# Kernel optimization log

Hardware: AMD Instinct MI355X
Metric: run time of the kernel (lower is better)

The kernel has to match this reference:

```python
import jax, jax.numpy as jnp
import numpy as np

STD = 0.5      # wrapper's self.std used as the noise sampling std
EPS = 1e-12    # BERT LayerNorm eps
NOISE_SEED = 42


def setup_inputs() -> dict:
    key = jax.random.key(0)
    ks = jax.random.split(key, 8)
    B, S, H, V, P, T = 32, 512, 768, 30522, 512, 2
    return {
        "input_ids": jax.random.randint(ks[0], (B, S), 0, V, dtype=jnp.int32),
        "token_type_ids": jnp.zeros((B, S), dtype=jnp.int32),
        "importance_scores": jax.random.uniform(ks[1], (B, S), dtype=jnp.float32),
        "word_emb": jax.random.normal(ks[2], (V, H), dtype=jnp.float32) * 0.02,
        "pos_emb": jax.random.normal(ks[3], (P, H), dtype=jnp.float32) * 0.02,
        "type_emb": jax.random.normal(ks[4], (T, H), dtype=jnp.float32) * 0.02,
        "ln_gamma": jnp.ones((H,), dtype=jnp.float32),
        "ln_beta": jnp.zeros((H,), dtype=jnp.float32),
    }


def _layernorm(x, g, b):
    mu = x.mean(-1, keepdims=True)
    var = ((x - mu) ** 2).mean(-1, keepdims=True)
    return (x - mu) * jax.lax.rsqrt(var + EPS) * g + b


def reference(input_ids, token_type_ids, importance_scores, word_emb, pos_emb,
              type_emb, ln_gamma, ln_beta):
    B, S = input_ids.shape
    # BERT embeddings: word + position + token_type, then LayerNorm (dropout=eval/no-op)
    emb = word_emb[input_ids] + pos_emb[:S][None, :, :] + type_emb[token_type_ids]
    x = _layernorm(emb, ln_gamma, ln_beta)  # [B,S,H]

    # min-max normalize importance scores per sequence (inf handled as in original)
    smax = importance_scores.max(axis=1, keepdims=True)
    tmp = jnp.where(jnp.isinf(importance_scores), 99.0, importance_scores)
    smin = tmp.min(axis=1, keepdims=True)
    norm = (importance_scores - smin) / (smax - smin)
    norm = jnp.where(importance_scores.sum() == 0, importance_scores, norm)

    finite = jnp.isfinite(importance_scores)
    score = jnp.where(finite, norm, 0.0)      # -inf positions masked out below
    score = score.at[:, 0].set(1.0)           # CLS token forced to importance 1
    mask = finite.at[:, 0].set(True)

    # soft_suff: sigma = 1 - importance; noise ~ N(0, STD); x += noise * sigma * x
    sigma = (1.0 - score) * mask.astype(x.dtype)          # [B,S]
    noise = jax.random.normal(jax.random.key(NOISE_SEED), x.shape, dtype=x.dtype) * STD
    x = x + noise * sigma[:, :, None] * jax.lax.stop_gradient(x)
    return x
```

## Files before the change

kernel.cpp:

```cpp
#include <hip/hip_runtime.h>
#include <hip/hip_bf16.h>
#include <math.h>

#define Hh   768
#define Ss   512
#define Bb   32
#define NTOK (Bb * Ss)
#define NTOT (NTOK * Hh)

__device__ __forceinline__ void tfr(unsigned &x0, unsigned &x1, int r) {
  x0 += x1;
  x1 = (x1 << r) | (x1 >> (32 - r));
  x1 ^= x0;
}

__device__ __forceinline__ uint2 threefry_0_42(unsigned x0, unsigned x1) {
  const unsigned ks0 = 0u, ks1 = 42u, ks2 = 0x1BD11BF0u;
  x0 += ks0; x1 += ks1;
  tfr(x0, x1, 13); tfr(x0, x1, 15); tfr(x0, x1, 26); tfr(x0, x1, 6);
  x0 += ks1; x1 += ks2 + 1u;
  tfr(x0, x1, 17); tfr(x0, x1, 29); tfr(x0, x1, 16); tfr(x0, x1, 24);
  x0 += ks2; x1 += ks0 + 2u;
  tfr(x0, x1, 13); tfr(x0, x1, 15); tfr(x0, x1, 26); tfr(x0, x1, 6);
  x0 += ks0; x1 += ks1 + 3u;
  tfr(x0, x1, 17); tfr(x0, x1, 29); tfr(x0, x1, 16); tfr(x0, x1, 24);
  x0 += ks1; x1 += ks2 + 4u;
  tfr(x0, x1, 13); tfr(x0, x1, 15); tfr(x0, x1, 26); tfr(x0, x1, 6);
  x0 += ks2; x1 += ks0 + 5u;
  return make_uint2(x0, x1);
}

__device__ __forceinline__ float erfinv_xla(float x) {
  float w = -log1pf(-x * x);
  float p;
  if (w < 5.0f) {
    w = w - 2.5f;
    p = 2.81022636e-08f;
    p = fmaf(p, w, 3.43273939e-07f);
    p = fmaf(p, w, -3.5233877e-06f);
    p = fmaf(p, w, -4.39150654e-06f);
    p = fmaf(p, w, 0.00021858087f);
    p = fmaf(p, w, -0.00125372503f);
    p = fmaf(p, w, -0.00417768164f);
    p = fmaf(p, w, 0.246640727f);
    p = fmaf(p, w, 1.50140941f);
  } else {
    w = sqrtf(w) - 3.0f;
    p = -0.000200214257f;
    p = fmaf(p, w, 0.000100950558f);
    p = fmaf(p, w, 0.00134934322f);
    p = fmaf(p, w, -0.00367342844f);
    p = fmaf(p, w, 0.00573950773f);
    p = fmaf(p, w, -0.0076224613f);
    p = fmaf(p, w, 0.00943887047f);
    p = fmaf(p, w, 1.00167406f);
    p = fmaf(p, w, 2.83297682f);
  }
  return p * x;
}

__device__ __forceinline__ float noise_at(unsigned i) {
  uint2 r = threefry_0_42(0u, i);
  unsigned bits = r.x ^ r.y;
  float f = __uint_as_float((bits >> 9) | 0x3F800000u) - 1.0f;
  const float LO = -0.99999994f;
  float u = fmaxf(LO, f * 2.0f + LO);
  return 1.41421354f * erfinv_xla(u) * 0.5f;
}

__global__ __launch_bounds__(512) void row_stats_kernel(
    const float* __restrict__ imp, float* __restrict__ ws) {
  int b = blockIdx.x;
  int tid = threadIdx.x;
  float v = imp[b * Ss + tid];
  float vmax = v;
  float vmin = isinf(v) ? 99.0f : v;
  float vsum = v;
  for (int o = 32; o > 0; o >>= 1) {
    vmax = fmaxf(vmax, __shfl_down(vmax, o));
    vmin = fminf(vmin, __shfl_down(vmin, o));
    vsum += __shfl_down(vsum, o);
  }
  __shared__ float smax[8], smin[8], ssum[8];
  int wave = tid >> 6, lane = tid & 63;
  if (lane == 0) { smax[wave] = vmax; smin[wave] = vmin; ssum[wave] = vsum; }
  __syncthreads();
  if (tid == 0) {
    float a = smax[0], m = smin[0], c = ssum[0];
    for (int w = 1; w < 8; ++w) {
      a = fmaxf(a, smax[w]); m = fminf(m, smin[w]); c += ssum[w];
    }
    ws[b] = a; ws[32 + b] = m; ws[64 + b] = c;
  }
}

__global__ __launch_bounds__(256) void bert_embed_ln_noise_kernel(
    const int* __restrict__ ids, const int* __restrict__ tts,
    const float* __restrict__ imp,
    const float* __restrict__ wemb, const float* __restrict__ pemb,
    const float* __restrict__ temb, const float* __restrict__ gamma,
    const float* __restrict__ beta, const float* __restrict__ stats,
    float* __restrict__ out) {
  const int t = blockIdx.x;
  const int b = t >> 9;
  const int s = t & 511;
  const int tid = threadIdx.x;

  const int id = ids[t];
  const int tt = tts[t];
  const float* wr = wemb + (size_t)id * Hh;
  const float* pr = pemb + (size_t)s * Hh;
  const float* tr = temb + (size_t)tt * Hh;

  float e0 = wr[tid]       + pr[tid]       + tr[tid];
  float e1 = wr[tid + 256] + pr[tid + 256] + tr[tid + 256];
  float e2 = wr[tid + 512] + pr[tid + 512] + tr[tid + 512];

  __shared__ float red[4];
  __shared__ float sh_sigma;
  const int wave = tid >> 6, lane = tid & 63;

  float ps = e0 + e1 + e2;
  for (int o = 32; o > 0; o >>= 1) ps += __shfl_down(ps, o);
  if (lane == 0) red[wave] = ps;
  __syncthreads();
  const float mu = (red[0] + red[1] + red[2] + red[3]) * (1.0f / Hh);
  __syncthreads();

  const float d0 = e0 - mu, d1 = e1 - mu, d2 = e2 - mu;
  float pv = d0 * d0 + d1 * d1 + d2 * d2;
  for (int o = 32; o > 0; o >>= 1) pv += __shfl_down(pv, o);
  if (lane == 0) red[wave] = pv;

  if (tid == 0) {
    float total = 0.0f;
    for (int w = 0; w < 32; ++w) total += stats[64 + w];
    const float score = imp[t];
    float sig = 0.0f;
    if (s != 0) {
      const bool fin = isfinite(score);
      const float mx = stats[b], mn = stats[32 + b];
      const float val = (total == 0.0f) ? score : (score - mn) / (mx - mn);
      const float sc = fin ? val : 0.0f;
      sig = fin ? (1.0f - sc) : 0.0f;
    }
    sh_sigma = sig;
  }
  __syncthreads();
  const float var = (red[0] + red[1] + red[2] + red[3]) * (1.0f / Hh);
  const float rstd = rsqrtf(var + 1e-12f);
  const float sig = sh_sigma;

  const float y0 = d0 * rstd * gamma[tid]       + beta[tid];
  const float y1 = d1 * rstd * gamma[tid + 256] + beta[tid + 256];
  const float y2 = d2 * rstd * gamma[tid + 512] + beta[tid + 512];

  const unsigned base = (unsigned)t * Hh;
  const float n0 = noise_at(base + tid);
  const float n1 = noise_at(base + tid + 256);
  const float n2 = noise_at(base + tid + 512);

  out[base + tid]       = fmaf(n0 * sig, y0, y0);
  out[base + tid + 256] = fmaf(n1 * sig, y1, y1);
  out[base + tid + 512] = fmaf(n2 * sig, y2, y2);
}

extern "C" void kernel_launch(void* const* d_in, const int* in_sizes, int n_in,
                              void* d_out, int out_size, void* d_ws, size_t ws_size,
                              hipStream_t stream) {
  const int*   ids   = (const int*)d_in[0];
  const int*   tts   = (const int*)d_in[1];
  const float* imp   = (const float*)d_in[2];
  const float* wemb  = (const float*)d_in[3];
  const float* pemb  = (const float*)d_in[4];
  const float* temb  = (const float*)d_in[5];
  const float* gamma = (const float*)d_in[6];
  const float* beta  = (const float*)d_in[7];
  float* out   = (float*)d_out;
  float* stats = (float*)d_ws;

  row_stats_kernel<<<Bb, Ss, 0, stream>>>(imp, stats);
  bert_embed_ln_noise_kernel<<<NTOK, 256, 0, stream>>>(
      ids, tts, imp, wemb, pemb, temb, gamma, beta, stats, out);
}
```

Baseline: 197.4 us.

## Vectorize embedding LN kernel with float4, 192 threads, hoisted noise generation

Each thread now handles four contiguous hidden elements through float4 loads and stores, with 192 threads per token block instead of 256. The Threefry noise and erfinv are computed before the reductions so they can overlap the memory latency. Threefry is specialised for key 0, the log1p is replaced by the fast __logf, and the sqrt(2)*std scale is folded into sigma. The fast log may change noise values slightly versus the XLA reference, and the 3-wave block shape changes occupancy.

Measured after the change: 173.6 us. 12.1% less time.

```diff
diff --git a/kernel.cpp b/kernel.cpp
--- a/kernel.cpp
+++ b/kernel.cpp
@@ -1,12 +1,11 @@
 #include <hip/hip_runtime.h>
-#include <hip/hip_bf16.h>
 #include <math.h>
 
 #define Hh   768
 #define Ss   512
 #define Bb   32
 #define NTOK (Bb * Ss)
-#define NTOT (NTOK * Hh)
+#define NT   192
 
 __device__ __forceinline__ void tfr(unsigned &x0, unsigned &x1, int r) {
   x0 += x1;
@@ -14,27 +13,30 @@
   x1 ^= x0;
 }
 
-__device__ __forceinline__ uint2 threefry_0_42(unsigned x0, unsigned x1) {
-  const unsigned ks0 = 0u, ks1 = 42u, ks2 = 0x1BD11BF0u;
-  x0 += ks0; x1 += ks1;
-  tfr(x0, x1, 13); tfr(x0, x1, 15); tfr(x0, x1, 26); tfr(x0, x1, 6);
+__device__ __forceinline__ unsigned tf_bits_0_42(unsigned ctr) {
+  const unsigned ks1 = 42u, ks2 = 0x1BD11BF0u;
+  unsigned x0 = 0u, x1 = ctr + ks1;
+  tfr(x0,x1,13); tfr(x0,x1,15); tfr(x0,x1,26); tfr(x0,x1,6);
   x0 += ks1; x1 += ks2 + 1u;
-  tfr(x0, x1, 17); tfr(x0, x1, 29); tfr(x0, x1, 16); tfr(x0, x1, 24);
-  x0 += ks2; x1 += ks0 + 2u;
-  tfr(x0, x1, 13); tfr(x0, x1, 15); tfr(x0, x1, 26); tfr(x0, x1, 6);
-  x0 += ks0; x1 += ks1 + 3u;
-  tfr(x0, x1, 17); tfr(x0, x1, 29); tfr(x0, x1, 16); tfr(x0, x1, 24);
+  tfr(x0,x1,17); tfr(x0,x1,29); tfr(x0,x1,16); tfr(x0,x1,24);
+  x0 += ks2; x1 += 2u;
+  tfr(x0,x1,13); tfr(x0,x1,15); tfr(x0,x1,26); tfr(x0,x1,6);
+  x1 += ks1 + 3u;
+  tfr(x0,x1,17); tfr(x0,x1,29); tfr(x0,x1,16); tfr(x0,x1,24);
   x0 += ks1; x1 += ks2 + 4u;
-  tfr(x0, x1, 13); tfr(x0, x1, 15); tfr(x0, x1, 26); tfr(x0, x1, 6);
-  x0 += ks2; x1 += ks0 + 5u;
-  return make_uint2(x0, x1);
+  tfr(x0,x1,13); tfr(x0,x1,15); tfr(x0,x1,26); tfr(x0,x1,6);
+  x0 += ks2; x1 += 5u;
+  return x0 ^ x1;
 }
 
-__device__ __forceinline__ float erfinv_xla(float x) {
-  float w = -log1pf(-x * x);
+__device__ __forceinline__ float erfinv_bits(unsigned bits) {
+  float f = __uint_as_float((bits >> 9) | 0x3F800000u) - 1.0f;
+  const float LO = -0.99999994f;
+  float x = fmaxf(LO, fmaf(f, 2.0f, LO));
+  float w = -__logf(fmaf(-x, x, 1.0f));
   float p;
   if (w < 5.0f) {
-    w = w - 2.5f;
+    w -= 2.5f;
     p = 2.81022636e-08f;
     p = fmaf(p, w, 3.43273939e-07f);
     p = fmaf(p, w, -3.5233877e-06f);
@@ -57,15 +59,6 @@
     p = fmaf(p, w, 2.83297682f);
   }
   return p * x;
-}
-
-__device__ __forceinline__ float noise_at(unsigned i) {
-  uint2 r = threefry_0_42(0u, i);
-  unsigned bits = r.x ^ r.y;
-  float f = __uint_as_float((bits >> 9) | 0x3F800000u) - 1.0f;
-  const float LO = -0.99999994f;
-  float u = fmaxf(LO, f * 2.0f + LO);
-  return 1.41421354f * erfinv_xla(u) * 0.5f;
 }
 
 __global__ __launch_bounds__(512) void row_stats_kernel(
@@ -94,7 +87,7 @@
   }
 }
 
-__global__ __launch_bounds__(256) void bert_embed_ln_noise_kernel(
+__global__ __launch_bounds__(NT) void bert_embed_ln_noise_kernel(
     const int* __restrict__ ids, const int* __restrict__ tts,
     const float* __restrict__ imp,
     const float* __restrict__ wemb, const float* __restrict__ pemb,
@@ -108,29 +101,41 @@
 
   const int id = ids[t];
   const int tt = tts[t];
-  const float* wr = wemb + (size_t)id * Hh;
-  const float* pr = pemb + (size_t)s * Hh;
-  const float* tr = temb + (size_t)tt * Hh;
+  const float4 wv = ((const float4*)(wemb + (size_t)id * Hh))[tid];
+  const float4 pv = ((const float4*)(pemb + (size_t)s  * Hh))[tid];
+  const float4 tv = ((const float4*)(temb + (size_t)tt * Hh))[tid];
 
-  float e0 = wr[tid]       + pr[tid]       + tr[tid];
-  float e1 = wr[tid + 256] + pr[tid + 256] + tr[tid + 256];
-  float e2 = wr[tid + 512] + pr[tid + 512] + tr[tid + 512];
+  const float e0 = wv.x + pv.x + tv.x;
+  const float e1 = wv.y + pv.y + tv.y;
+  const float e2 = wv.z + pv.z + tv.z;
+  const float e3 = wv.w + pv.w + tv.w;
 
-  __shared__ float red[4];
-  __shared__ float sh_sigma;
+  const unsigned base = (unsigned)t * Hh + 4u * (unsigned)tid;
+  const unsigned r0 = tf_bits_0_42(base);
+  const unsigned r1 = tf_bits_0_42(base + 1u);
+  const unsigned r2 = tf_bits_0_42(base + 2u);
+  const unsigned r3 = tf_bits_0_42(base + 3u);
+  const float v0 = erfinv_bits(r0);
+  const float v1 = erfinv_bits(r1);
+  const float v2 = erfinv_bits(r2);
+  const float v3 = erfinv_bits(r3);
+
+  __shared__ float redm[3], redv[3];
+  __shared__ float sh_ssc;
   const int wave = tid >> 6, lane = tid & 63;
 
-  float ps = e0 + e1 + e2;
-  for (int o = 32; o > 0; o >>= 1) ps += __shfl_down(ps, o);
-  if (lane == 0) red[wave] = ps;
+  float ps = (e0 + e1) + (e2 + e3);
+  #pragma unroll
+  for (int o = 1; o < 64; o <<= 1) ps += __shfl_xor(ps, o);
+  if (lane == 0) redm[wave] = ps;
   __syncthreads();
-  const float mu = (red[0] + red[1] + red[2] + red[3]) * (1.0f / Hh);
-  __syncthreads();
+  const float mu = (redm[0] + redm[1] + redm[2]) * (1.0f / Hh);
 
-  const float d0 = e0 - mu, d1 = e1 - mu, d2 = e2 - mu;
-  float pv = d0 * d0 + d1 * d1 + d2 * d2;
-  for (int o = 32; o > 0; o >>= 1) pv += __shfl_down(pv, o);
-  if (lane == 0) red[wave] = pv;
+  const float d0 = e0 - mu, d1 = e1 - mu, d2 = e2 - mu, d3 = e3 - mu;
+  float pvv = (d0 * d0 + d1 * d1) + (d2 * d2 + d3 * d3);
+  #pragma unroll
+  for (int o = 1; o < 64; o <<= 1) pvv += __shfl_xor(pvv, o);
+  if (lane == 0) redv[wave] = pvv;
 
   if (tid == 0) {
     float total = 0.0f;
@@ -141,28 +146,28 @@
       const bool fin = isfinite(score);
       const float mx = stats[b], mn = stats[32 + b];
       const float val = (total == 0.0f) ? score : (score - mn) / (mx - mn);
-      const float sc = fin ? val : 0.0f;
-      sig = fin ? (1.0f - sc) : 0.0f;
+      sig = fin ? (1.0f - val) : 0.0f;
     }
-    sh_sigma = sig;
+    sh_ssc = sig * 0.70710677f;
   }
   __syncthreads();
-  const float var = (red[0] + red[1] + red[2] + red[3]) * (1.0f / Hh);
+  const float var = (redv[0] + redv[1] + redv[2]) * (1.0f / Hh);
   const float rstd = rsqrtf(var + 1e-12f);
-  const float sig = sh_sigma;
+  const float ssc = sh_ssc;
 
-  const float y0 = d0 * rstd * gamma[tid]       + beta[tid];
-  const float y1 = d1 * rstd * gamma[tid + 256] + beta[tid + 256];
-  const float y2 = d2 * rstd * gamma[tid + 512] + beta[tid + 512];
+  const float4 g4 = ((const float4*)gamma)[tid];
+  const float4 b4 = ((const float4*)beta)[tid];
+  const float y0 = fmaf(d0 * rstd, g4.x, b4.x);
+  const float y1 = fmaf(d1 * rstd, g4.y, b4.y);
+  const float y2 = fmaf(d2 * rstd, g4.z, b4.z);
+  const float y3 = fmaf(d3 * rstd, g4.w, b4.w);
 
-  const unsigned base = (unsigned)t * Hh;
-  const float n0 = noise_at(base + tid);
-  const float n1 = noise_at(base + tid + 256);
-  const float n2 = noise_at(base + tid + 512);
-
-  out[base + tid]       = fmaf(n0 * sig, y0, y0);
-  out[base + tid + 256] = fmaf(n1 * sig, y1, y1);
-  out[base + tid + 512] = fmaf(n2 * sig, y2, y2);
+  float4 o4;
+  o4.x = fmaf(v0 * ssc, y0, y0);
+  o4.y = fmaf(v1 * ssc, y1, y1);
+  o4.z = fmaf(v2 * ssc, y2, y2);
+  o4.w = fmaf(v3 * ssc, y3, y3);
+  ((float4*)(out + (size_t)t * Hh))[tid] = o4;
 }
 
 extern "C" void kernel_launch(void* const* d_in, const int* in_sizes, int n_in,
@@ -180,6 +185,6 @@
   float* stats = (float*)d_ws;
 
   row_stats_kernel<<<Bb, Ss, 0, stream>>>(imp, stats);
-  bert_embed_ln_noise_kernel<<<NTOK, 256, 0, stream>>>(
+  bert_embed_ln_noise_kernel<<<NTOK, NT, 0, stream>>>(
       ids, tts, imp, wemb, pemb, temb, gamma, beta, stats, out);
 }
```
